# Kernel tuning notes

Hardware: AMD Instinct MI355X
Metric: run time of the kernel (lower is better)

## Reference

```python
import jax, jax.numpy as jnp
import numpy as np

OUT_CAPS_NUM = 16
OUT_CAPS_DIM = 512
ITER_NUM = 3
EPS = 1e-7


def setup_inputs() -> dict:
    key = jax.random.key(0)
    k_x, k_w = jax.random.split(key)
    x = jax.random.normal(k_x, (32, 128, 1024), dtype=jnp.float32)
    # xavier_normal-ish scale so tanh is not saturated
    W = jax.random.normal(k_w, (1024, OUT_CAPS_NUM * OUT_CAPS_DIM), dtype=jnp.float32) * 0.02
    return {"x": x, "W": W}


def _squash(S):
    # squash in source = divide by sqrt(||S||^2 + eps) (unit-ish norm)
    scale = jnp.sqrt(jnp.sum(S * S, axis=-1, keepdims=True) + EPS)
    return S / scale


def reference(x, W):
    b, s, _ = x.shape
    # caps_uhat: (b, s, out_caps_num, out_caps_dim)
    caps_uhat = jnp.tanh(jnp.einsum("bsd,dk->bsk", x, W)).reshape(
        b, s, OUT_CAPS_NUM, OUT_CAPS_DIM
    )
    B = jnp.zeros((b, s, OUT_CAPS_NUM), dtype=x.dtype)
    C_list = []
    B_logits = B
    V = None
    for _ in range(ITER_NUM):
        B_logits = B
        C = jax.nn.softmax(B, axis=2)          # (b, s, n)
        C_list.append(C)
        S = jnp.einsum("bsn,bsnd->bnd", C, caps_uhat)  # weighted sum over seq
        V = _squash(S)                          # (b, n, d)
        # agreement update: sum over caps dim
        B = jnp.einsum("bsnd,bnd->bsn", caps_uhat, V) + B
    C_ret = jnp.stack(C_list)                   # (iter, b, s, n)
    return (V, C_ret, B_logits)
```

## Files before the change

### kernel.cpp

```cpp
#include <hip/hip_runtime.h>
#include <math.h>

typedef float f32x4 __attribute__((ext_vector_type(4)));
typedef float f32x2 __attribute__((ext_vector_type(2)));
typedef int   i32x4 __attribute__((ext_vector_type(4)));
typedef unsigned short u16;
typedef u16 u16x4 __attribute__((ext_vector_type(4)));

#define BDIM 32
#define SDIM 128
#define NCAPS 16
#define DCAPS 512
#define MG 4096
#define NG 8192
#define KG 1024

__device__ __forceinline__ u16 f2bf(float f) {
  unsigned u = __builtin_bit_cast(unsigned, f);
  u += 0x7fffu + ((u >> 16) & 1u);
  return (u16)(u >> 16);
}
__device__ __forceinline__ float bflo(unsigned u) {
  return __builtin_bit_cast(float, u << 16);
}
__device__ __forceinline__ float bfhi(unsigned u) {
  return __builtin_bit_cast(float, u & 0xffff0000u);
}

__device__ __forceinline__ void gload16(const void* g, void* l) {
  __builtin_amdgcn_global_load_lds(
      (const __attribute__((address_space(1))) void*)g,
      (__attribute__((address_space(3))) void*)l, 16, 0, 0);
}

__device__ __forceinline__ f32x4 mfma_bf16(i32x4 a, i32x4 b, f32x4 c) {
  asm("v_mfma_f32_16x16x32_bf16 %0, %1, %2, %0" : "+v"(c) : "v"(a), "v"(b));
  return c;
}

__global__ __launch_bounds__(256) void k_convx(const float* __restrict__ x,
                                               u16* __restrict__ xb) {
  int i = blockIdx.x * 256 + threadIdx.x;
  f32x4 v = ((const f32x4*)x)[i];
  u16x4 r = { f2bf(v.x), f2bf(v.y), f2bf(v.z), f2bf(v.w) };
  ((u16x4*)xb)[i] = r;
}

__global__ __launch_bounds__(256) void k_transW(const float* __restrict__ W,
                                                u16* __restrict__ wt) {
  __shared__ float tile[32][33];
  const int n0 = blockIdx.x * 32;
  const int k0 = blockIdx.y * 32;
  const int tx = threadIdx.x & 31;
  const int ty = threadIdx.x >> 5;
#pragma unroll
  for (int r = 0; r < 32; r += 8)
    tile[ty + r][tx] = W[(size_t)(k0 + ty + r) * NG + n0 + tx];
  __syncthreads();
#pragma unroll
  for (int r = 0; r < 32; r += 8)
    wt[(size_t)(n0 + ty + r) * KG + k0 + tx] = f2bf(tile[tx][ty + r]);
}

__global__ __launch_bounds__(256) void k_init(float* __restrict__ C0,
                                              float* __restrict__ Bws) {
  int i = blockIdx.x * 256 + threadIdx.x;
  f32x4 c = { 0.0625f, 0.0625f, 0.0625f, 0.0625f };
  f32x4 z = {};
  ((f32x4*)C0)[i] = c;
  ((f32x4*)Bws)[i] = z;
}

__global__ __launch_bounds__(256) void k_gemm_tanh(const u16* __restrict__ xb,
                                                   const u16* __restrict__ wt,
                                                   u16* __restrict__ uhat) {
  __shared__ u16 As[128 * 32];
  __shared__ u16 Bs[128 * 32];
  const int m0 = blockIdx.y * 128;
  const int n0 = blockIdx.x * 128;
  const int t = threadIdx.x;
  const int lane = t & 63;
  const int wave = t >> 6;
  const int wr = (wave >> 1) * 64;
  const int wc = (wave & 1) * 64;
  f32x4 acc[4][4] = {};

  const int r0 = t >> 2;
  const int r1 = (256 + t) >> 2;
  const int c0 = (t & 3) * 8;
  const u16* ga0 = xb + (size_t)(m0 + r0) * KG + c0;
  const u16* ga1 = xb + (size_t)(m0 + r1) * KG + c0;
  const u16* gb0 = wt + (size_t)(n0 + r0) * KG + c0;
  const u16* gb1 = wt + (size_t)(n0 + r1) * KG + c0;
  u16* la0 = &As[t * 8];
  u16* la1 = &As[(256 + t) * 8];
  u16* lb0 = &Bs[t * 8];
  u16* lb1 = &Bs[(256 + t) * 8];

  const int am = lane & 15;
  const int ak = (lane >> 4) * 8;

  for (int kt = 0; kt < KG; kt += 32) {
    gload16(ga0 + kt, la0);
    gload16(ga1 + kt, la1);
    gload16(gb0 + kt, lb0);
    gload16(gb1 + kt, lb1);
    __syncthreads();
    i32x4 af[4], bf[4];
#pragma unroll
    for (int mi = 0; mi < 4; ++mi)
      af[mi] = *(const i32x4*)&As[(wr + mi * 16 + am) * 32 + ak];
#pragma unroll
    for (int ni = 0; ni < 4; ++ni)
      bf[ni] = *(const i32x4*)&Bs[(wc + ni * 16 + am) * 32 + ak];
#pragma unroll
    for (int mi = 0; mi < 4; ++mi)
#pragma unroll
      for (int ni = 0; ni < 4; ++ni)
        acc[mi][ni] = mfma_bf16(af[mi], bf[ni], acc[mi][ni]);
    __syncthreads();
  }

  const int crow0 = (lane >> 4) * 4;
  const int ccol = lane & 15;
#pragma unroll
  for (int mi = 0; mi < 4; ++mi)
#pragma unroll
    for (int ni = 0; ni < 4; ++ni)
#pragma unroll
      for (int j = 0; j < 4; ++j) {
        int row = m0 + wr + mi * 16 + crow0 + j;
        int col = n0 + wc + ni * 16 + ccol;
        uhat[(size_t)row * NG + col] = f2bf(tanhf(acc[mi][ni][j]));
      }
}

__global__ __launch_bounds__(256) void k_spass(const u16* __restrict__ uhat,
                                               const float* __restrict__ C,
                                               float* __restrict__ V) {
  const int n = blockIdx.x;
  const int b = blockIdx.y;
  const int t = threadIdx.x;
  __shared__ float cl[128];
  __shared__ float red[4];
  if (t < 128) cl[t] = C[((size_t)b * 128 + t) * 16 + n];
  __syncthreads();
  const u16* up = uhat + (((size_t)b * 128) * 16 + n) * 512 + 2 * t;
  float a0 = 0.f, a1 = 0.f;
#pragma unroll 4
  for (int s = 0; s < 128; ++s) {
    unsigned u = *(const unsigned*)(up + (size_t)s * 8192);
    float c = cl[s];
    a0 = fmaf(c, bflo(u), a0);
    a1 = fmaf(c, bfhi(u), a1);
  }
  float ss = a0 * a0 + a1 * a1;
#pragma unroll
  for (int m = 1; m < 64; m <<= 1) ss += __shfl_xor(ss, m);
  if ((t & 63) == 0) red[t >> 6] = ss;
  __syncthreads();
  float tot = red[0] + red[1] + red[2] + red[3];
  float r = 1.0f / sqrtf(tot + 1e-7f);
  f32x2 vv = { a0 * r, a1 * r };
  *(f32x2*)(V + ((size_t)b * 16 + n) * 512 + 2 * t) = vv;
}

__global__ __launch_bounds__(256) void k_bupdate(const u16* __restrict__ uhat,
                                                 const float* __restrict__ V,
                                                 float* __restrict__ Bws,
                                                 float* __restrict__ Cnext,
                                                 float* __restrict__ Blog) {
  const int bs = blockIdx.x;
  const int b = bs >> 7;
  const int t = threadIdx.x;
  const int n = t >> 4;
  const int j = t & 15;
  const u16* up = uhat + ((size_t)bs * 16 + n) * 512 + j * 32;
  const float* vp = V + ((size_t)b * 16 + n) * 512 + j * 32;
  float dot = 0.f;
#pragma unroll
  for (int q = 0; q < 4; ++q) {
    i32x4 u = *(const i32x4*)(up + q * 8);
    f32x4 v0 = *(const f32x4*)(vp + q * 8);
    f32x4 v1 = *(const f32x4*)(vp + q * 8 + 4);
    dot = fmaf(bflo(u.x), v0.x, dot);
    dot = fmaf(bfhi(u.x), v0.y, dot);
    dot = fmaf(bflo(u.y), v0.z, dot);
    dot = fmaf(bfhi(u.y), v0.w, dot);
    dot = fmaf(bflo(u.z), v1.x, dot);
    dot = fmaf(bfhi(u.z), v1.y, dot);
    dot = fmaf(bflo(u.w), v1.z, dot);
    dot = fmaf(bfhi(u.w), v1.w, dot);
  }
#pragma unroll
  for (int m = 1; m < 16; m <<= 1) dot += __shfl_xor(dot, m);
  __shared__ float bl[16];
  if (j == 0) bl[n] = Bws[(size_t)bs * 16 + n] + dot;
  __syncthreads();
  if (t < 16) {
    float mx = -1e30f;
#pragma unroll
    for (int k2 = 0; k2 < 16; ++k2) mx = fmaxf(mx, bl[k2]);
    float e = expf(bl[t] - mx);
    float sum = 0.f;
#pragma unroll
    for (int k2 = 0; k2 < 16; ++k2) sum += expf(bl[k2] - mx);
    size_t o = (size_t)bs * 16 + t;
    Cnext[o] = e / sum;
    float bn = bl[t];
    Bws[o] = bn;
    if (Blog) Blog[o] = bn;
  }
}

extern "C" void kernel_launch(void* const* d_in, const int* in_sizes, int n_in,
                              void* d_out, int out_size, void* d_ws, size_t ws_size,
                              hipStream_t stream) {
  const float* x = (const float*)d_in[0];
  const float* W = (const float*)d_in[1];
  float* out = (float*)d_out;
  float* Vout = out;
  float* Cout = out + 262144;
  float* Blog = out + 262144 + 196608;

  char* ws = (char*)d_ws;
  u16* uhat = (u16*)ws;
  u16* xb   = (u16*)(ws + 67108864);
  u16* wt   = (u16*)(ws + 67108864 + 8388608);
  float* Vws = (float*)(ws + 92274688);
  float* Bws = (float*)(ws + 93323264);

  k_convx<<<4096, 256, 0, stream>>>(x, xb);
  k_transW<<<dim3(256, 32), 256, 0, stream>>>(W, wt);
  k_init<<<64, 256, 0, stream>>>(Cout, Bws);
  k_gemm_tanh<<<dim3(64, 32), 256, 0, stream>>>(xb, wt, uhat);
  k_spass<<<dim3(16, 32), 256, 0, stream>>>(uhat, Cout, Vws);
  k_bupdate<<<4096, 256, 0, stream>>>(uhat, Vws, Bws, Cout + 65536, nullptr);
  k_spass<<<dim3(16, 32), 256, 0, stream>>>(uhat, Cout + 65536, Vws);
  k_bupdate<<<4096, 256, 0, stream>>>(uhat, Vws, Bws, Cout + 2 * 65536, Blog);
  k_spass<<<dim3(16, 32), 256, 0, stream>>>(uhat, Cout + 2 * 65536, Vout);
}
```

Baseline: 287.6 us.

## Deepen GEMM K-step, use fast tanh, and widen spass loads with split-seq reduction

The GEMM now loads two 32-wide K slices per barrier pair, halving the number of syncs per K sweep. The accurate tanhf in the epilogue is replaced with an exp/reciprocal formula. The S-pass kernel reads 16-byte vectors, splits the sequence across four waves, and reduces the partial sums through shared memory before squashing. This gives wider memory transactions and fewer dependent FMAs per thread, at the cost of extra LDS and slightly lower tanh precision.

```diff
diff --git a/kernel.cpp b/kernel.cpp
--- a/kernel.cpp
+++ b/kernel.cpp
@@ -7,11 +7,6 @@
 typedef unsigned short u16;
 typedef u16 u16x4 __attribute__((ext_vector_type(4)));
 
-#define BDIM 32
-#define SDIM 128
-#define NCAPS 16
-#define DCAPS 512
-#define MG 4096
 #define NG 8192
 #define KG 1024
 
@@ -36,6 +31,13 @@
 __device__ __forceinline__ f32x4 mfma_bf16(i32x4 a, i32x4 b, f32x4 c) {
   asm("v_mfma_f32_16x16x32_bf16 %0, %1, %2, %0" : "+v"(c) : "v"(a), "v"(b));
   return c;
+}
+
+__device__ __forceinline__ float fast_tanh(float x) {
+  float ax = fabsf(x);
+  float e = __expf(-2.0f * ax);
+  float r = (1.0f - e) * __frcp_rn(1.0f + e);
+  return copysignf(r, x);
 }
 
 __global__ __launch_bounds__(256) void k_convx(const float* __restrict__ x,
@@ -74,8 +76,8 @@
 __global__ __launch_bounds__(256) void k_gemm_tanh(const u16* __restrict__ xb,
                                                    const u16* __restrict__ wt,
                                                    u16* __restrict__ uhat) {
-  __shared__ u16 As[128 * 32];
-  __shared__ u16 Bs[128 * 32];
+  __shared__ u16 As[2][128 * 32];
+  __shared__ u16 Bs[2][128 * 32];
   const int m0 = blockIdx.y * 128;
   const int n0 = blockIdx.x * 128;
   const int t = threadIdx.x;
@@ -86,38 +88,41 @@
   f32x4 acc[4][4] = {};
 
   const int r0 = t >> 2;
-  const int r1 = (256 + t) >> 2;
+  const int r1 = 64 + (t >> 2);
   const int c0 = (t & 3) * 8;
   const u16* ga0 = xb + (size_t)(m0 + r0) * KG + c0;
   const u16* ga1 = xb + (size_t)(m0 + r1) * KG + c0;
   const u16* gb0 = wt + (size_t)(n0 + r0) * KG + c0;
   const u16* gb1 = wt + (size_t)(n0 + r1) * KG + c0;
-  u16* la0 = &As[t * 8];
-  u16* la1 = &As[(256 + t) * 8];
-  u16* lb0 = &Bs[t * 8];
-  u16* lb1 = &Bs[(256 + t) * 8];
 
   const int am = lane & 15;
   const int ak = (lane >> 4) * 8;
 
-  for (int kt = 0; kt < KG; kt += 32) {
-    gload16(ga0 + kt, la0);
-    gload16(ga1 + kt, la1);
-    gload16(gb0 + kt, lb0);
-    gload16(gb1 + kt, lb1);
+  for (int kt = 0; kt < KG; kt += 64) {
+#pragma unroll
+    for (int kh = 0; kh < 2; ++kh) {
+      const int ko = kt + kh * 32;
+      gload16(ga0 + ko, &As[kh][t * 8]);
+      gload16(ga1 + ko, &As[kh][(256 + t) * 8]);
+      gload16(gb0 + ko, &Bs[kh][t * 8]);
+      gload16(gb1 + ko, &Bs[kh][(256 + t) * 8]);
+    }
     __syncthreads();
-    i32x4 af[4], bf[4];
-#pragma unroll
-    for (int mi = 0; mi < 4; ++mi)
-      af[mi] = *(const i32x4*)&As[(wr + mi * 16 + am) * 32 + ak];
-#pragma unroll
-    for (int ni = 0; ni < 4; ++ni)
-      bf[ni] = *(const i32x4*)&Bs[(wc + ni * 16 + am) * 32 + ak];
-#pragma unroll
-    for (int mi = 0; mi < 4; ++mi)
+#pragma unroll
+    for (int kh = 0; kh < 2; ++kh) {
+      i32x4 af[4], bf[4];
+#pragma unroll
+      for (int mi = 0; mi < 4; ++mi)
+        af[mi] = *(const i32x4*)&As[kh][(wr + mi * 16 + am) * 32 + ak];
 #pragma unroll
       for (int ni = 0; ni < 4; ++ni)
-        acc[mi][ni] = mfma_bf16(af[mi], bf[ni], acc[mi][ni]);
+        bf[ni] = *(const i32x4*)&Bs[kh][(wc + ni * 16 + am) * 32 + ak];
+#pragma unroll
+      for (int mi = 0; mi < 4; ++mi)
+#pragma unroll
+        for (int ni = 0; ni < 4; ++ni)
+          acc[mi][ni] = mfma_bf16(af[mi], bf[ni], acc[mi][ni]);
+    }
     __syncthreads();
   }
 
@@ -131,7 +136,7 @@
       for (int j = 0; j < 4; ++j) {
         int row = m0 + wr + mi * 16 + crow0 + j;
         int col = n0 + wc + ni * 16 + ccol;
-        uhat[(size_t)row * NG + col] = f2bf(tanhf(acc[mi][ni][j]));
+        uhat[(size_t)row * NG + col] = f2bf(fast_tanh(acc[mi][ni][j]));
       }
 }
 
@@ -141,28 +146,47 @@
   const int n = blockIdx.x;
   const int b = blockIdx.y;
   const int t = threadIdx.x;
+  const int g = t >> 6;
+  const int dl = t & 63;
   __shared__ float cl[128];
-  __shared__ float red[4];
+  __shared__ float Sred[4][512];
   if (t < 128) cl[t] = C[((size_t)b * 128 + t) * 16 + n];
   __syncthreads();
-  const u16* up = uhat + (((size_t)b * 128) * 16 + n) * 512 + 2 * t;
-  float a0 = 0.f, a1 = 0.f;
+
+  const u16* up = uhat + (((size_t)b * 128) * 16 + n) * 512 + dl * 8;
+  float a[8] = {};
 #pragma unroll 4
-  for (int s = 0; s < 128; ++s) {
-    unsigned u = *(const unsigned*)(up + (size_t)s * 8192);
+  for (int i = 0; i < 32; ++i) {
+    const int s = g + i * 4;
+    i32x4 u = *(const i32x4*)(up + (size_t)s * NG);
     float c = cl[s];
-    a0 = fmaf(c, bflo(u), a0);
-    a1 = fmaf(c, bfhi(u), a1);
-  }
-  float ss = a0 * a0 + a1 * a1;
-#pragma unroll
-  for (int m = 1; m < 64; m <<= 1) ss += __shfl_xor(ss, m);
-  if ((t & 63) == 0) red[t >> 6] = ss;
-  __syncthreads();
-  float tot = red[0] + red[1] + red[2] + red[3];
-  float r = 1.0f / sqrtf(tot + 1e-7f);
-  f32x2 vv = { a0 * r, a1 * r };
-  *(f32x2*)(V + ((size_t)b * 16 + n) * 512 + 2 * t) = vv;
+    a[0] = fmaf(c, bflo(u.x), a[0]); a[1] = fmaf(c, bfhi(u.x), a[1]);
+    a[2] = fmaf(c, bflo(u.y), a[2]); a[3] = fmaf(c, bfhi(u.y), a[3]);
+    a[4] = fmaf(c, bflo(u.z), a[4]); a[5] = fmaf(c, bfhi(u.z), a[5]);
+    a[6] = fmaf(c, bflo(u.w), a[6]); a[7] = fmaf(c, bfhi(u.w), a[7]);
+  }
+#pragma unroll
+  for (int e = 0; e < 8; ++e) Sred[g][dl * 8 + e] = a[e];
+  __syncthreads();
+
+  if (g == 0) {
+    float S[8];
+    float ss = 0.f;
+#pragma unroll
+    for (int e = 0; e < 8; ++e) {
+      int d = dl * 8 + e;
+      S[e] = Sred[0][d] + Sred[1][d] + Sred[2][d] + Sred[3][d];
+      ss = fmaf(S[e], S[e], ss);
+    }
+#pragma unroll
+    for (int m = 1; m < 64; m <<= 1) ss += __shfl_xor(ss, m);
+    float r = rsqrtf(ss + 1e-7f);
+    float* vp = V + ((size_t)b * 16 + n) * 512 + dl * 8;
+    f32x4 v0 = { S[0] * r, S[1] * r, S[2] * r, S[3] * r };
+    f32x4 v1 = { S[4] * r, S[5] * r, S[6] * r, S[7] * r };
+    *(f32x4*)vp = v0;
+    *(f32x4*)(vp + 4) = v1;
+  }
 }
 
 __global__ __launch_bounds__(256) void k_bupdate(const u16* __restrict__ uhat,
```

Measured after the change: 272.9 us. -5.1%, faster.
